# Kernel optimization log

Hardware: AMD Instinct MI355X
Metric: run time of the kernel (lower is better)

## Reference

```python
import jax, jax.numpy as jnp
import numpy as np

DROP_P = 0.5
DROP_KEY = jax.random.key(42)  # fixed key: deterministic dropout mask


def setup_inputs() -> dict:
    key = jax.random.key(0)
    k1, k2, k3 = jax.random.split(key, 3)
    B, H, S, D = 2, 16, 2048, 128
    x1 = jax.random.normal(k1, (B, H, S, D), dtype=jnp.float32)
    x2 = jax.random.normal(k2, (B, H, S, D), dtype=jnp.float32)
    # broadcastable per-head divisor; offset to keep it away from zero
    x3 = jax.random.uniform(k3, (B, H, 1, 1), dtype=jnp.float32) + 1.0
    return {"x1": x1, "x2": x2, "x3": x3}


def reference(x1, x2, x3):
    # v1 = x1 @ x2^T  -> [B,H,S,S]; v2 = v1 / x3 (broadcast divisor)
    scores = jnp.einsum('bhqd,bhkd->bhqk', x1, x2) / x3
    # v3 = softmax over last dim
    probs = jax.nn.softmax(scores, axis=-1)
    # v4 = dropout(p=0.5), training=True semantics: mask and rescale by 1/(1-p)
    keep = jax.random.bernoulli(DROP_KEY, 1.0 - DROP_P, probs.shape)
    probs = jnp.where(keep, probs / (1.0 - DROP_P), 0.0)
    # v5 = v4 @ x1 (note: values are x1, not a separate V); v6 = v5 + x2 residual
    out = jnp.einsum('bhqk,bhkd->bhqd', probs, x1) + x2
    return out
```

## Files before the change

kernel.cpp:

```cpp
#include <hip/hip_runtime.h>
#include <math.h>


constexpr int Sc = 2048, Dc = 128;
constexpr int BQ = 128, BK = 64, NTILES = Sc / BK;
constexpr int LDK = 132;
constexpr int LDP = 68;
constexpr int LDOE = 68;

typedef short bf16x8 __attribute__((ext_vector_type(8)));
typedef float f32x16 __attribute__((ext_vector_type(16)));
union U8 { uint4 u; bf16x8 v; };

__device__ __forceinline__ unsigned rotl32(unsigned x, int r) {
  return (x << r) | (x >> (32 - r));
}

__device__ __forceinline__ void tf2x32(unsigned x0, unsigned x1,
                                       unsigned &o0, unsigned &o1) {
  const unsigned ks0 = 0u, ks1 = 42u;
  const unsigned ks2 = 0x1BD11BDAu ^ 0u ^ 42u;
  x0 += ks0; x1 += ks1;
#define TFR(r) { x0 += x1; x1 = rotl32(x1, r); x1 ^= x0; }
  TFR(13) TFR(15) TFR(26) TFR(6)
  x0 += ks1; x1 += ks2 + 1u;
  TFR(17) TFR(29) TFR(16) TFR(24)
  x0 += ks2; x1 += ks0 + 2u;
  TFR(13) TFR(15) TFR(26) TFR(6)
  x0 += ks0; x1 += ks1 + 3u;
  TFR(17) TFR(29) TFR(16) TFR(24)
  x0 += ks1; x1 += ks2 + 4u;
  TFR(13) TFR(15) TFR(26) TFR(6)
  x0 += ks2; x1 += ks0 + 5u;
#undef TFR
  o0 = x0; o1 = x1;
}

__device__ __forceinline__ unsigned keepbit(unsigned idx) {
  unsigned o0, o1; tf2x32(0u, idx, o0, o1);
  return (((o0 ^ o1) >> 31) ^ 1u);
}

__device__ __forceinline__ unsigned pk2(float a, float b) {
  unsigned ua = __float_as_uint(a), ub = __float_as_uint(b);
  ua += 0x7fffu + ((ua >> 16) & 1u);
  ub += 0x7fffu + ((ub >> 16) & 1u);
  return (ua >> 16) | (ub & 0xffff0000u);
}

__global__ __launch_bounds__(256, 2)
void attn_mfma(const float* __restrict__ x1, const float* __restrict__ x2,
               const float* __restrict__ x3, float* __restrict__ out) {
  __shared__ alignas(16) char smem[64*LDK*2 + 128*64*2 + 4*32*LDP*2];
  ushort* Ks = (ushort*)smem;
  ushort* Vt = (ushort*)(smem + 64*LDK*2);
  ushort* Ps = (ushort*)(smem + 64*LDK*2 + 128*64*2);
  float*  Os = (float*)smem;

  const int tid = threadIdx.x;
  const int wave = tid >> 6, lane = tid & 63;
  const int r = lane & 31, h = lane >> 5;
  const int blk = blockIdx.x;
  const int bh = blk & 31, qt = blk >> 5;

  const float* X1 = x1 + (size_t)bh * Sc * Dc;
  const float* X2 = x2 + (size_t)bh * Sc * Dc;
  float* outp = out + (size_t)bh * Sc * Dc;
  const float inv_div = 1.0f / x3[bh];

  const int qrow = qt * BQ + wave * 32 + r;
  const unsigned row_base = (unsigned)(bh * Sc + qrow) * (unsigned)Sc;

  bf16x8 qf[8];
  {
    const float4* qsrc = (const float4*)(X1 + (size_t)qrow * Dc);
#pragma unroll
    for (int ch = 0; ch < 8; ++ch) {
      float4 f0 = qsrc[ch*4 + h*2 + 0];
      float4 f1 = qsrc[ch*4 + h*2 + 1];
      U8 cv; cv.u = uint4{pk2(f0.x,f0.y), pk2(f0.z,f0.w), pk2(f1.x,f1.y), pk2(f1.z,f1.w)};
      qf[ch] = cv.v;
    }
  }

  f32x16 o0 = {}, o1 = {}, o2 = {}, o3 = {};
  float m_run = -INFINITY, l_run = 0.0f;

  for (int t = 0; t < NTILES; ++t) {
    __syncthreads();
    {
      const float4* ksrc = (const float4*)(X2 + (size_t)t * BK * Dc);
#pragma unroll
      for (int it = 0; it < 8; ++it) {
        int f = tid + 256*it;
        int key = f >> 5, c = f & 31;
        float4 kv = ksrc[f];
        uint2 w; w.x = pk2(kv.x, kv.y); w.y = pk2(kv.z, kv.w);
        *(uint2*)&Ks[key*LDK + c*4] = w;
      }
    }
    {
      const float* vbase = X1 + (size_t)t * BK * Dc;
#pragma unroll
      for (int it = 0; it < 2; ++it) {
        int g = tid + 256*it;
        int c = g & 31, kb = g >> 5;
        const float4* vs = (const float4*)(vbase + (size_t)(kb*4) * Dc) + c;
        float4 a0 = vs[0], a1 = vs[32], a2 = vs[64], a3 = vs[96];
        float e0[4] = {a0.x,a0.y,a0.z,a0.w};
        float e1[4] = {a1.x,a1.y,a1.z,a1.w};
        float e2[4] = {a2.x,a2.y,a2.z,a2.w};
        float e3[4] = {a3.x,a3.y,a3.z,a3.w};
#pragma unroll
        for (int i = 0; i < 4; ++i) {
          int d = c*4 + i;
          int pkb = (kb + c + 4*i) & 15;
          uint2 w; w.x = pk2(e0[i], e1[i]); w.y = pk2(e2[i], e3[i]);
          *(uint2*)&Vt[d*64 + pkb*4] = w;
        }
      }
    }
    __syncthreads();

    f32x16 s0v = {}, s1v = {};
    {
      const ushort* ka0 = &Ks[(     r)*LDK + h*8];
      const ushort* ka1 = &Ks[(32 + r)*LDK + h*8];
#pragma unroll
      for (int ch = 0; ch < 8; ++ch) {
        uint2 u00 = *(const uint2*)&ka0[ch*16];
        uint2 u01 = *(const uint2*)&ka0[ch*16 + 4];
        uint2 u10 = *(const uint2*)&ka1[ch*16];
        uint2 u11 = *(const uint2*)&ka1[ch*16 + 4];
        U8 c0; c0.u = uint4{u00.x,u00.y,u01.x,u01.y};
        U8 c1; c1.u = uint4{u10.x,u10.y,u11.x,u11.y};
        s0v = __builtin_amdgcn_mfma_f32_32x32x16_bf16(c0.v, qf[ch], s0v, 0,0,0);
        s1v = __builtin_amdgcn_mfma_f32_32x32x16_bf16(c1.v, qf[ch], s1v, 0,0,0);
      }
    }

    float sv0[16], sv1[16];
    float mx = -INFINITY;
#pragma unroll
    for (int i = 0; i < 16; ++i) {
      sv0[i] = s0v[i] * inv_div; sv1[i] = s1v[i] * inv_div;
      mx = fmaxf(mx, fmaxf(sv0[i], sv1[i]));
    }
    mx = fmaxf(mx, __shfl_xor(mx, 32));
    float m_new = fmaxf(m_run, mx);
    float alpha = __expf(m_run - m_new);
    float ls = 0.0f;
#pragma unroll
    for (int i = 0; i < 16; ++i) {
      sv0[i] = __expf(sv0[i] - m_new); ls += sv0[i];
      sv1[i] = __expf(sv1[i] - m_new); ls += sv1[i];
    }
    ls += __shfl_xor(ls, 32);
    l_run = l_run * alpha + ls;
    m_run = m_new;

    ushort* pw = Ps + wave*(32*LDP) + r*LDP;
#pragma unroll
    for (int mt = 0; mt < 2; ++mt)
#pragma unroll
      for (int rg = 0; rg < 4; ++rg) {
        int k0 = mt*32 + rg*8 + h*4;
        const float* sp = mt ? sv1 : sv0;
        uint2 w; w.x = pk2(sp[rg*4+0], sp[rg*4+1]); w.y = pk2(sp[rg*4+2], sp[rg*4+3]);
        *(uint2*)&pw[k0] = w;
      }

    {
      unsigned idx0 = row_base + (unsigned)(t * BK) + (unsigned)(h * 4);
#pragma unroll 1
      for (int g = 0; g < 8; ++g) {
        int kk = (g >> 2)*32 + (g & 3)*8;
        int k0 = kk + h*4;
        unsigned ib = idx0 + (unsigned)kk;
        uint2 w = *(uint2*)&pw[k0];
        unsigned m0 = (keepbit(ib+0) ? 0x0000ffffu : 0u) | (keepbit(ib+1) ? 0xffff0000u : 0u);
        unsigned m1 = (keepbit(ib+2) ? 0x0000ffffu : 0u) | (keepbit(ib+3) ? 0xffff0000u : 0u);
        w.x &= m0; w.y &= m1;
        *(uint2*)&pw[k0] = w;
      }
    }

#pragma unroll
    for (int i = 0; i < 16; ++i) { o0[i]*=alpha; o1[i]*=alpha; o2[i]*=alpha; o3[i]*=alpha; }
#pragma unroll
    for (int ch = 0; ch < 4; ++ch) {
      uint2 b0 = *(const uint2*)&pw[ch*16 + h*8];
      uint2 b1 = *(const uint2*)&pw[ch*16 + h*8 + 4];
      U8 bf; bf.u = uint4{b0.x,b0.y,b1.x,b1.y};
      int kb0 = ch*4 + h*2;
#pragma unroll
      for (int dmt = 0; dmt < 4; ++dmt) {
        int d = dmt*32 + r;
        int sw = (d >> 2) + 4*(d & 3);
        int p0 = (kb0     + sw) & 15;
        int p1 = (kb0 + 1 + sw) & 15;
        uint2 aa = *(const uint2*)&Vt[d*64 + p0*4];
        uint2 bb = *(const uint2*)&Vt[d*64 + p1*4];
        U8 af; af.u = uint4{aa.x,aa.y,bb.x,bb.y};
        f32x16& oc = dmt==0 ? o0 : dmt==1 ? o1 : dmt==2 ? o2 : o3;
        oc = __builtin_amdgcn_mfma_f32_32x32x16_bf16(af.v, bf.v, oc, 0,0,0);
      }
    }
  }

  const float invl = 2.0f / l_run;
#pragma unroll
  for (int half = 0; half < 2; ++half) {
    __syncthreads();
    {
      float* ow = Os + (size_t)(wave*32 + r) * LDOE;
#pragma unroll
      for (int dm = 0; dm < 2; ++dm) {
        const int dmt = half*2 + dm;
        const f32x16& oc = dmt==0 ? o0 : dmt==1 ? o1 : dmt==2 ? o2 : o3;
#pragma unroll
        for (int rg = 0; rg < 4; ++rg) {
          int dd = dm*32 + rg*8 + h*4;
          float2 w0{oc[rg*4+0]*invl, oc[rg*4+1]*invl};
          float2 w1{oc[rg*4+2]*invl, oc[rg*4+3]*invl};
          *(float2*)&ow[dd]     = w0;
          *(float2*)&ow[dd + 2] = w1;
        }
      }
    }
    __syncthreads();
#pragma unroll
    for (int it = 0; it < 8; ++it) {
      int f = tid + 256*it;
      int q = f >> 4, cc = f & 15;
      const float4 ov = *(const float4*)&Os[q*LDOE + cc*4];
      size_t goff = (size_t)(qt*BQ + q) * Dc + half*64 + cc*4;
      const float4 xv = *(const float4*)&X2[goff];
      float4 res{ov.x+xv.x, ov.y+xv.y, ov.z+xv.z, ov.w+xv.w};
      *(float4*)&outp[goff] = res;
    }
  }
}

extern "C" void kernel_launch(void* const* d_in, const int* in_sizes, int n_in,
                              void* d_out, int out_size, void* d_ws, size_t ws_size,
                              hipStream_t stream) {
  const float* x1 = (const float*)d_in[0];
  const float* x2 = (const float*)d_in[1];
  const float* x3 = (const float*)d_in[2];
  float* out = (float*)d_out;
  dim3 grid(32 * (Sc / BQ));
  attn_mfma<<<grid, 256, 0, stream>>>(x1, x2, x3, out);
}
```

Measured before the change: 443.0 us.

## Prepack K/V into bf16 MFMA fragment layout and rewrite attention with 16x16 MFMA

```diff
diff --git a/kernel.cpp b/kernel.cpp
--- a/kernel.cpp
+++ b/kernel.cpp
@@ -3,13 +3,12 @@
 
 
 constexpr int Sc = 2048, Dc = 128;
-constexpr int BQ = 128, BK = 64, NTILES = Sc / BK;
-constexpr int LDK = 132;
-constexpr int LDP = 68;
-constexpr int LDOE = 68;
+constexpr int BK = 64, NT = Sc / BK;
+constexpr int KS_B = 16384, VS_B = 16384;
+constexpr int PS_B = 8192;
 
 typedef short bf16x8 __attribute__((ext_vector_type(8)));
-typedef float f32x16 __attribute__((ext_vector_type(16)));
+typedef float f32x4 __attribute__((ext_vector_type(4)));
 union U8 { uint4 u; bf16x8 v; };
 
 __device__ __forceinline__ unsigned rotl32(unsigned x, int r) {
@@ -36,209 +35,196 @@
   o0 = x0; o1 = x1;
 }
 
-__device__ __forceinline__ unsigned keepbit(unsigned idx) {
-  unsigned o0, o1; tf2x32(0u, idx, o0, o1);
-  return (((o0 ^ o1) >> 31) ^ 1u);
-}
-
-__device__ __forceinline__ unsigned pk2(float a, float b) {
-  unsigned ua = __float_as_uint(a), ub = __float_as_uint(b);
-  ua += 0x7fffu + ((ua >> 16) & 1u);
-  ub += 0x7fffu + ((ub >> 16) & 1u);
-  return (ua >> 16) | (ub & 0xffff0000u);
-}
-
-__global__ __launch_bounds__(256, 2)
-void attn_mfma(const float* __restrict__ x1, const float* __restrict__ x2,
-               const float* __restrict__ x3, float* __restrict__ out) {
-  __shared__ alignas(16) char smem[64*LDK*2 + 128*64*2 + 4*32*LDP*2];
-  ushort* Ks = (ushort*)smem;
-  ushort* Vt = (ushort*)(smem + 64*LDK*2);
-  ushort* Ps = (ushort*)(smem + 64*LDK*2 + 128*64*2);
-  float*  Os = (float*)smem;
-
-  const int tid = threadIdx.x;
-  const int wave = tid >> 6, lane = tid & 63;
-  const int r = lane & 31, h = lane >> 5;
-  const int blk = blockIdx.x;
-  const int bh = blk & 31, qt = blk >> 5;
-
-  const float* X1 = x1 + (size_t)bh * Sc * Dc;
-  const float* X2 = x2 + (size_t)bh * Sc * Dc;
-  float* outp = out + (size_t)bh * Sc * Dc;
-  const float inv_div = 1.0f / x3[bh];
-
-  const int qrow = qt * BQ + wave * 32 + r;
+__device__ __forceinline__ unsigned pk2rn(float a, float b) {
+  return __builtin_amdgcn_perm(__float_as_uint(b) + 0x8000u,
+                               __float_as_uint(a) + 0x8000u, 0x07060302u);
+}
+
+__device__ __forceinline__ void gload16(const void* g, void* l) {
+  __builtin_amdgcn_global_load_lds(
+      (const __attribute__((address_space(1))) void*)g,
+      (__attribute__((address_space(3))) void*)l, 16, 0, 0);
+}
+
+__global__ __launch_bounds__(256)
+void prepack(const float* __restrict__ x1, const float* __restrict__ x2,
+             uint4* __restrict__ Kb, uint4* __restrict__ Vt) {
+  __shared__ ushort Vl[64 * 68];
+  const int tid = threadIdx.x, blk = blockIdx.x;
+  const int half = blk & 1, tile = blk >> 1;
+  const float* x2t = x2 + (size_t)tile * 8192;
+  const float* x1t = x1 + (size_t)tile * 8192;
+  uint4* KbT = Kb + (size_t)tile * 1024;
+  uint4* VtT = Vt + (size_t)tile * 1024;
+#pragma unroll
+  for (int it = 0; it < 2; ++it) {
+    int u = half * 512 + it * 256 + tid;
+    int mt = u >> 8, c = (u >> 6) & 3, g = (u >> 4) & 3, m16 = u & 15;
+    const float4* s = (const float4*)(x2t + (mt * 16 + m16) * 128 + c * 32 + g * 8);
+    float4 f0 = s[0], f1 = s[1];
+    KbT[u] = uint4{pk2rn(f0.x, f0.y), pk2rn(f0.z, f0.w),
+                   pk2rn(f1.x, f1.y), pk2rn(f1.z, f1.w)};
+  }
+#pragma unroll
+  for (int it = 0; it < 4; ++it) {
+    int f = it * 256 + tid;
+    int row = f >> 4, c4 = f & 15;
+    float4 v = *(const float4*)(x1t + row * 128 + half * 64 + c4 * 4);
+    *(uint2*)&Vl[row * 68 + c4 * 4] = uint2{pk2rn(v.x, v.y), pk2rn(v.z, v.w)};
+  }
+  __syncthreads();
+#pragma unroll
+  for (int it = 0; it < 2; ++it) {
+    int ul = it * 256 + tid;
+    int dtl = ul >> 7, c = (ul >> 6) & 1, g = (ul >> 4) & 3, m16 = ul & 15;
+    int dl = dtl * 16 + m16, k0 = c * 32 + g * 8;
+    unsigned w[4];
+#pragma unroll
+    for (int p = 0; p < 4; ++p) {
+      unsigned lo = Vl[(k0 + 2 * p) * 68 + dl];
+      unsigned hi = Vl[(k0 + 2 * p + 1) * 68 + dl];
+      w[p] = lo | (hi << 16);
+    }
+    VtT[(((dtl + half * 4) * 2 + c) * 4 + g) * 16 + m16] = uint4{w[0], w[1], w[2], w[3]};
+  }
+}
+
+__global__ __launch_bounds__(256, 4)
+void attn4(const uint4* __restrict__ Kb, const uint4* __restrict__ Vt,
+           const float* __restrict__ x1, const float* __restrict__ x2,
+           const float* __restrict__ x3, float* __restrict__ out) {
+  __shared__ uint4 smemv[(KS_B + VS_B + PS_B) / 16];
+  char* smem = (char*)smemv;
+  ushort* Ps = (ushort*)(smem + KS_B + VS_B);
+  float* Os = (float*)smem;
+
+  const int tid = threadIdx.x, wave = tid >> 6, lane = tid & 63;
+  const int g = lane >> 4, q = lane & 15;
+  const int blk = blockIdx.x, bh = blk & 31, qt = blk >> 5;
+
+  const float* X1 = x1 + (size_t)bh * (Sc * Dc);
+  const float* X2 = x2 + (size_t)bh * (Sc * Dc);
+  float* outp = out + (size_t)bh * (Sc * Dc);
+  const float cl2 = (1.0f / x3[bh]) * 1.4426950408889634f;
+
+  const int qrow = qt * 64 + wave * 16 + q;
   const unsigned row_base = (unsigned)(bh * Sc + qrow) * (unsigned)Sc;
 
-  bf16x8 qf[8];
+  bf16x8 qf[4];
   {
     const float4* qsrc = (const float4*)(X1 + (size_t)qrow * Dc);
 #pragma unroll
-    for (int ch = 0; ch < 8; ++ch) {
-      float4 f0 = qsrc[ch*4 + h*2 + 0];
-      float4 f1 = qsrc[ch*4 + h*2 + 1];
-      U8 cv; cv.u = uint4{pk2(f0.x,f0.y), pk2(f0.z,f0.w), pk2(f1.x,f1.y), pk2(f1.z,f1.w)};
-      qf[ch] = cv.v;
-    }
-  }
-
-  f32x16 o0 = {}, o1 = {}, o2 = {}, o3 = {};
-  float m_run = -INFINITY, l_run = 0.0f;
-
-  for (int t = 0; t < NTILES; ++t) {
+    for (int c = 0; c < 4; ++c) {
+      float4 f0 = qsrc[c * 8 + g * 2], f1 = qsrc[c * 8 + g * 2 + 1];
+      U8 cv; cv.u = uint4{pk2rn(f0.x, f0.y), pk2rn(f0.z, f0.w),
+                          pk2rn(f1.x, f1.y), pk2rn(f1.z, f1.w)};
+      qf[c] = cv.v;
+    }
+  }
+
+  f32x4 o[8];
+#pragma unroll
+  for (int i = 0; i < 8; ++i) o[i] = f32x4{0.f, 0.f, 0.f, 0.f};
+  float l_run = 0.0f;
+  const int tbase = bh * 32;
+  ushort* pw = Ps + wave * 1024 + q * 64;
+
+  for (int t = 0; t < NT; ++t) {
     __syncthreads();
     {
-      const float4* ksrc = (const float4*)(X2 + (size_t)t * BK * Dc);
-#pragma unroll
-      for (int it = 0; it < 8; ++it) {
-        int f = tid + 256*it;
-        int key = f >> 5, c = f & 31;
-        float4 kv = ksrc[f];
-        uint2 w; w.x = pk2(kv.x, kv.y); w.y = pk2(kv.z, kv.w);
-        *(uint2*)&Ks[key*LDK + c*4] = w;
+      const char* kg = (const char*)(Kb + (size_t)(tbase + t) * 1024);
+      const char* vg = (const char*)(Vt + (size_t)(tbase + t) * 1024);
+#pragma unroll
+      for (int j = 0; j < 4; ++j) {
+        int off = j * 4096 + wave * 1024 + lane * 16;
+        gload16(kg + off, smem + off);
+        gload16(vg + off, smem + KS_B + off);
       }
     }
+    __syncthreads();
+
+    f32x4 s0 = {}, s1 = {}, s2 = {}, s3 = {};
+#pragma unroll
+    for (int c = 0; c < 4; ++c) {
+      U8 a0; a0.u = *(const uint4*)(smem + ((0 * 4 + c) * 64 + lane) * 16);
+      U8 a1; a1.u = *(const uint4*)(smem + ((1 * 4 + c) * 64 + lane) * 16);
+      U8 a2; a2.u = *(const uint4*)(smem + ((2 * 4 + c) * 64 + lane) * 16);
+      U8 a3; a3.u = *(const uint4*)(smem + ((3 * 4 + c) * 64 + lane) * 16);
+      s0 = __builtin_amdgcn_mfma_f32_16x16x32_bf16(a0.v, qf[c], s0, 0, 0, 0);
+      s1 = __builtin_amdgcn_mfma_f32_16x16x32_bf16(a1.v, qf[c], s1, 0, 0, 0);
+      s2 = __builtin_amdgcn_mfma_f32_16x16x32_bf16(a2.v, qf[c], s2, 0, 0, 0);
+      s3 = __builtin_amdgcn_mfma_f32_16x16x32_bf16(a3.v, qf[c], s3, 0, 0, 0);
+    }
+
+    float pr[16];
+    float ls = 0.0f;
+#pragma unroll
+    for (int i = 0; i < 4; ++i) { pr[i]      = __builtin_amdgcn_exp2f(s0[i] * cl2); ls += pr[i]; }
+#pragma unroll
+    for (int i = 0; i < 4; ++i) { pr[4 + i]  = __builtin_amdgcn_exp2f(s1[i] * cl2); ls += pr[4 + i]; }
+#pragma unroll
+    for (int i = 0; i < 4; ++i) { pr[8 + i]  = __builtin_amdgcn_exp2f(s2[i] * cl2); ls += pr[8 + i]; }
+#pragma unroll
+    for (int i = 0; i < 4; ++i) { pr[12 + i] = __builtin_amdgcn_exp2f(s3[i] * cl2); ls += pr[12 + i]; }
+    ls += __shfl_xor(ls, 16);
+    ls += __shfl_xor(ls, 32);
+    l_run += ls;
+
+    unsigned db = 0u;
     {
-      const float* vbase = X1 + (size_t)t * BK * Dc;
-#pragma unroll
-      for (int it = 0; it < 2; ++it) {
-        int g = tid + 256*it;
-        int c = g & 31, kb = g >> 5;
-        const float4* vs = (const float4*)(vbase + (size_t)(kb*4) * Dc) + c;
-        float4 a0 = vs[0], a1 = vs[32], a2 = vs[64], a3 = vs[96];
-        float e0[4] = {a0.x,a0.y,a0.z,a0.w};
-        float e1[4] = {a1.x,a1.y,a1.z,a1.w};
-        float e2[4] = {a2.x,a2.y,a2.z,a2.w};
-        float e3[4] = {a3.x,a3.y,a3.z,a3.w};
-#pragma unroll
-        for (int i = 0; i < 4; ++i) {
-          int d = c*4 + i;
-          int pkb = (kb + c + 4*i) & 15;
-          uint2 w; w.x = pk2(e0[i], e1[i]); w.y = pk2(e2[i], e3[i]);
-          *(uint2*)&Vt[d*64 + pkb*4] = w;
-        }
+      const unsigned ib = row_base + (unsigned)(t * 64) + (unsigned)(g * 4);
+#pragma unroll 4
+      for (unsigned j = 0; j < 16; ++j) {
+        unsigned key = ((j & 12u) << 2) | (j & 3u);
+        unsigned a, b;
+        tf2x32(0u, ib + key, a, b);
+        db |= ((a ^ b) >> 31) << j;
       }
     }
-    __syncthreads();
-
-    f32x16 s0v = {}, s1v = {};
-    {
-      const ushort* ka0 = &Ks[(     r)*LDK + h*8];
-      const ushort* ka1 = &Ks[(32 + r)*LDK + h*8];
-#pragma unroll
-      for (int ch = 0; ch < 8; ++ch) {
-        uint2 u00 = *(const uint2*)&ka0[ch*16];
-        uint2 u01 = *(const uint2*)&ka0[ch*16 + 4];
-        uint2 u10 = *(const uint2*)&ka1[ch*16];
-        uint2 u11 = *(const uint2*)&ka1[ch*16 + 4];
-        U8 c0; c0.u = uint4{u00.x,u00.y,u01.x,u01.y};
-        U8 c1; c1.u = uint4{u10.x,u10.y,u11.x,u11.y};
-        s0v = __builtin_amdgcn_mfma_f32_32x32x16_bf16(c0.v, qf[ch], s0v, 0,0,0);
-        s1v = __builtin_amdgcn_mfma_f32_32x32x16_bf16(c1.v, qf[ch], s1v, 0,0,0);
+
+#pragma unroll
+    for (int mt = 0; mt < 4; ++mt) {
+      float a0_ = ((db >> (mt * 4 + 0)) & 1u) ? 0.f : pr[mt * 4 + 0];
+      float a1_ = ((db >> (mt * 4 + 1)) & 1u) ? 0.f : pr[mt * 4 + 1];
+      float a2_ = ((db >> (mt * 4 + 2)) & 1u) ? 0.f : pr[mt * 4 + 2];
+      float a3_ = ((db >> (mt * 4 + 3)) & 1u) ? 0.f : pr[mt * 4 + 3];
+      *(uint2*)&pw[((mt * 4 + g) ^ q) * 4] = uint2{pk2rn(a0_, a1_), pk2rn(a2_, a3_)};
+    }
+
+#pragma unroll
+    for (int c2 = 0; c2 < 2; ++c2) {
+      int u0 = c2 * 8 + g * 2;
+      uint2 b0 = *(const uint2*)&pw[(u0 ^ q) * 4];
+      uint2 b1 = *(const uint2*)&pw[((u0 + 1) ^ q) * 4];
+      U8 bfr; bfr.u = uint4{b0.x, b0.y, b1.x, b1.y};
+#pragma unroll
+      for (int dt = 0; dt < 8; ++dt) {
+        U8 av; av.u = *(const uint4*)(smem + KS_B + ((dt * 2 + c2) * 64 + lane) * 16);
+        o[dt] = __builtin_amdgcn_mfma_f32_16x16x32_bf16(av.v, bfr.v, o[dt], 0, 0, 0);
       }
     }
-
-    float sv0[16], sv1[16];
-    float mx = -INFINITY;
-#pragma unroll
-    for (int i = 0; i < 16; ++i) {
-      sv0[i] = s0v[i] * inv_div; sv1[i] = s1v[i] * inv_div;
-      mx = fmaxf(mx, fmaxf(sv0[i], sv1[i]));
-    }
-    mx = fmaxf(mx, __shfl_xor(mx, 32));
-    float m_new = fmaxf(m_run, mx);
-    float alpha = __expf(m_run - m_new);
-    float ls = 0.0f;
-#pragma unroll
-    for (int i = 0; i < 16; ++i) {
-      sv0[i] = __expf(sv0[i] - m_new); ls += sv0[i];
-      sv1[i] = __expf(sv1[i] - m_new); ls += sv1[i];
-    }
-    ls += __shfl_xor(ls, 32);
-    l_run = l_run * alpha + ls;
-    m_run = m_new;
-
-    ushort* pw = Ps + wave*(32*LDP) + r*LDP;
-#pragma unroll
-    for (int mt = 0; mt < 2; ++mt)
-#pragma unroll
-      for (int rg = 0; rg < 4; ++rg) {
-        int k0 = mt*32 + rg*8 + h*4;
-        const float* sp = mt ? sv1 : sv0;
-        uint2 w; w.x = pk2(sp[rg*4+0], sp[rg*4+1]); w.y = pk2(sp[rg*4+2], sp[rg*4+3]);
-        *(uint2*)&pw[k0] = w;
-      }
-
-    {
-      unsigned idx0 = row_base + (unsigned)(t * BK) + (unsigned)(h * 4);
-#pragma unroll 1
-      for (int g = 0; g < 8; ++g) {
-        int kk = (g >> 2)*32 + (g & 3)*8;
-        int k0 = kk + h*4;
-        unsigned ib = idx0 + (unsigned)kk;
-        uint2 w = *(uint2*)&pw[k0];
-        unsigned m0 = (keepbit(ib+0) ? 0x0000ffffu : 0u) | (keepbit(ib+1) ? 0xffff0000u : 0u);
-        unsigned m1 = (keepbit(ib+2) ? 0x0000ffffu : 0u) | (keepbit(ib+3) ? 0xffff0000u : 0u);
-        w.x &= m0; w.y &= m1;
-        *(uint2*)&pw[k0] = w;
-      }
-    }
-
-#pragma unroll
-    for (int i = 0; i < 16; ++i) { o0[i]*=alpha; o1[i]*=alpha; o2[i]*=alpha; o3[i]*=alpha; }
-#pragma unroll
-    for (int ch = 0; ch < 4; ++ch) {
-      uint2 b0 = *(const uint2*)&pw[ch*16 + h*8];
-      uint2 b1 = *(const uint2*)&pw[ch*16 + h*8 + 4];
-      U8 bf; bf.u = uint4{b0.x,b0.y,b1.x,b1.y};
-      int kb0 = ch*4 + h*2;
-#pragma unroll
-      for (int dmt = 0; dmt < 4; ++dmt) {
-        int d = dmt*32 + r;
-        int sw = (d >> 2) + 4*(d & 3);
-        int p0 = (kb0     + sw) & 15;
-        int p1 = (kb0 + 1 + sw) & 15;
-        uint2 aa = *(const uint2*)&Vt[d*64 + p0*4];
-        uint2 bb = *(const uint2*)&Vt[d*64 + p1*4];
-        U8 af; af.u = uint4{aa.x,aa.y,bb.x,bb.y};
-        f32x16& oc = dmt==0 ? o0 : dmt==1 ? o1 : dmt==2 ? o2 : o3;
-        oc = __builtin_amdgcn_mfma_f32_32x32x16_bf16(af.v, bf.v, oc, 0,0,0);
-      }
-    }
   }
 
   const float invl = 2.0f / l_run;
-#pragma unroll
-  for (int half = 0; half < 2; ++half) {
-    __syncthreads();
-    {
-      float* ow = Os + (size_t)(wave*32 + r) * LDOE;
-#pragma unroll
-      for (int dm = 0; dm < 2; ++dm) {
-        const int dmt = half*2 + dm;
-        const f32x16& oc = dmt==0 ? o0 : dmt==1 ? o1 : dmt==2 ? o2 : o3;
-#pragma unroll
-        for (int rg = 0; rg < 4; ++rg) {
-          int dd = dm*32 + rg*8 + h*4;
-          float2 w0{oc[rg*4+0]*invl, oc[rg*4+1]*invl};
-          float2 w1{oc[rg*4+2]*invl, oc[rg*4+3]*invl};
-          *(float2*)&ow[dd]     = w0;
-          *(float2*)&ow[dd + 2] = w1;
-        }
-      }
-    }
-    __syncthreads();
-#pragma unroll
-    for (int it = 0; it < 8; ++it) {
-      int f = tid + 256*it;
-      int q = f >> 4, cc = f & 15;
-      const float4 ov = *(const float4*)&Os[q*LDOE + cc*4];
-      size_t goff = (size_t)(qt*BQ + q) * Dc + half*64 + cc*4;
-      const float4 xv = *(const float4*)&X2[goff];
-      float4 res{ov.x+xv.x, ov.y+xv.y, ov.z+xv.z, ov.w+xv.w};
-      *(float4*)&outp[goff] = res;
-    }
+  __syncthreads();
+  {
+    float* ow = Os + (size_t)(wave * 16 + q) * 132;
+#pragma unroll
+    for (int dt = 0; dt < 8; ++dt) {
+      int d = dt * 16 + g * 4;
+      *(float4*)&ow[d] = float4{o[dt][0] * invl, o[dt][1] * invl,
+                                o[dt][2] * invl, o[dt][3] * invl};
+    }
+  }
+  __syncthreads();
+#pragma unroll
+  for (int it = 0; it < 8; ++it) {
+    int f = it * 256 + tid;
+    int ql = f >> 5, c4 = f & 31;
+    float4 ov = *(const float4*)&Os[ql * 132 + c4 * 4];
+    size_t goff = (size_t)(qt * 64 + ql) * Dc + c4 * 4;
+    float4 xv = *(const float4*)&X2[goff];
+    *(float4*)&outp[goff] = float4{ov.x + xv.x, ov.y + xv.y, ov.z + xv.z, ov.w + xv.w};
   }
 }
 
@@ -249,6 +235,9 @@
   const float* x2 = (const float*)d_in[1];
   const float* x3 = (const float*)d_in[2];
   float* out = (float*)d_out;
-  dim3 grid(32 * (Sc / BQ));
-  attn_mfma<<<grid, 256, 0, stream>>>(x1, x2, x3, out);
-}
+  const size_t PREP = (size_t)1024 * 1024 * 16;
+  uint4* Kb = (uint4*)d_ws;
+  uint4* Vtg = (uint4*)((char*)d_ws + PREP);
+  prepack<<<2048, 256, 0, stream>>>(x1, x2, Kb, Vtg);
+  attn4<<<1024, 256, 0, stream>>>(Kb, Vtg, x1, x2, x3, out);
+}
```

Result: faster. 430.3 us (-2.9%).
